# Kernel tuning notes

Measured on AMD Instinct MI355X. Metric: run time of the kernel, lower is better.

Reference implementation:

```python
import jax, jax.numpy as jnp
import numpy as np

HEADS = 16
HEAD_DIM = 128
LAMBDA_INIT = 0.8
RMS_EPS = 1.1920928955078125e-07  # torch.finfo(float32).eps (RMSNorm eps=None default)


def setup_inputs() -> dict:
    key = jax.random.key(0)
    ks = jax.random.split(key, 9)
    b, s, d = 2, 2048, 2048
    x = jax.random.normal(ks[0], (b, s, d), dtype=jnp.float32)
    # torch Linear weights are (out_features, in_features); apply as x @ W.T
    wq = jax.random.normal(ks[1], (d, d), dtype=jnp.float32) * 0.02
    wk = jax.random.normal(ks[2], (d, d), dtype=jnp.float32) * 0.02
    wv = jax.random.normal(ks[3], (d, d), dtype=jnp.float32) * 0.02
    wo = jax.random.normal(ks[4], (d, d), dtype=jnp.float32) * 0.02
    # lambda vectors scaled small so exp(dot) stays finite
    lambda_q1 = jax.random.normal(ks[5], (HEAD_DIM,), dtype=jnp.float32) * 0.1
    lambda_q2 = jax.random.normal(ks[6], (HEAD_DIM,), dtype=jnp.float32) * 0.1
    lambda_k1 = jax.random.normal(ks[7], (HEAD_DIM,), dtype=jnp.float32) * 0.1
    lambda_k2 = jax.random.normal(ks[8], (HEAD_DIM,), dtype=jnp.float32) * 0.1
    return {"x": x, "wq": wq, "wk": wk, "wv": wv, "wo": wo,
            "lambda_q1": lambda_q1, "lambda_q2": lambda_q2,
            "lambda_k1": lambda_k1, "lambda_k2": lambda_k2}


def reference(x, wq, wk, wv, wo, lambda_q1, lambda_q2, lambda_k1, lambda_k2):
    b, s, d = x.shape
    h, hd = HEADS, HEAD_DIM
    # projections -> (b, h, s, hd)
    q = (x @ wq.T).reshape(b, s, h, hd).transpose(0, 2, 1, 3)
    k = (x @ wk.T).reshape(b, s, h, hd).transpose(0, 2, 1, 3)
    v = (x @ wv.T).reshape(b, s, h, hd).transpose(0, 2, 1, 3)
    q1, q2 = jnp.split(q, 2, axis=-1)
    k1, k2 = jnp.split(k, 2, axis=-1)
    # NOTE: source scales by sqrt(full head_dim), not the chunked dim
    scale = 1.0 / jnp.sqrt(jnp.float32(hd))
    a1 = jax.nn.softmax(jnp.einsum('bhqd,bhkd->bhqk', q1, k1) * scale, axis=-1)
    a2 = jax.nn.softmax(jnp.einsum('bhqd,bhkd->bhqk', q2, k2) * scale, axis=-1)
    lam = jnp.exp(jnp.dot(lambda_q1, lambda_k1)) - jnp.exp(jnp.dot(lambda_q2, lambda_k2)) + LAMBDA_INIT
    out = jnp.einsum('bhqk,bhkd->bhqd', a1 - lam * a2, v)  # (b,h,s,hd)
    # per-head RMSNorm (no affine) scaled by (1 - lambda_init)
    rms = jnp.sqrt(jnp.mean(out * out, axis=-1, keepdims=True) + RMS_EPS)
    normed = out / rms * (1.0 - LAMBDA_INIT)
    # faithful to torch: cat over heads on dim 1 -> (b, h*s, hd),
    # transpose(1,2) -> (b, hd, h*s), contiguous view -> (b, s, d)
    t = normed.reshape(b, h * s, hd).transpose(0, 2, 1).reshape(b, s, d)
    return t @ wo.T
```

## Files before the change

### kernel.cpp

```cpp
#include <hip/hip_runtime.h>
#include <hip/hip_bf16.h>
#include <cstdint>
#include <cstddef>

typedef __attribute__((ext_vector_type(8))) short short8;
typedef __attribute__((ext_vector_type(4))) float f4;
typedef __attribute__((ext_vector_type(4))) int i4;

#define MFMA16(a, b, c) __builtin_amdgcn_mfma_f32_16x16x32_bf16((a), (b), (c), 0, 0, 0)

__device__ __forceinline__ float bf2f(unsigned short u) {
    union { unsigned int i; float f; } v; v.i = ((unsigned int)u) << 16; return v.f;
}
__device__ __forceinline__ unsigned short f2bf(float f) {
    union { float f; unsigned int i; } v; v.f = f;
    unsigned int x = v.i;
    x += 0x7fffu + ((x >> 16) & 1u);
    return (unsigned short)(x >> 16);
}
__device__ __forceinline__ i4 pack8(const float* p) {
    f4 v0 = *(const f4*)p;
    f4 v1 = *(const f4*)(p + 4);
    unsigned int w0 = (unsigned int)f2bf(v0[0]) | ((unsigned int)f2bf(v0[1]) << 16);
    unsigned int w1 = (unsigned int)f2bf(v0[2]) | ((unsigned int)f2bf(v0[3]) << 16);
    unsigned int w2 = (unsigned int)f2bf(v1[0]) | ((unsigned int)f2bf(v1[1]) << 16);
    unsigned int w3 = (unsigned int)f2bf(v1[2]) | ((unsigned int)f2bf(v1[3]) << 16);
    i4 r; r[0] = (int)w0; r[1] = (int)w1; r[2] = (int)w2; r[3] = (int)w3; return r;
}

static constexpr int S = 2048;
static constexpr int D = 2048;
static constexpr int H = 16;
static constexpr int HD = 128;
static constexpr int B = 2;

__global__ void detect_kernel(const unsigned short* __restrict__ w,
                              const void* __restrict__ lq1, const void* __restrict__ lq2,
                              const void* __restrict__ lk1, const void* __restrict__ lk2,
                              int* __restrict__ ctrl) {
    const int lane = threadIdx.x;
    int hits = 0;
    for (int j = 0; j < 4; j++) {
        unsigned short u = w[lane * 4 + j];
        hits += (((u >> 7) & 0xFF) >= 134) ? 1 : 0;
    }
    for (int m = 1; m <= 32; m <<= 1) hits += __shfl_xor(hits, m, 64);
    const int flag = (hits >= 16) ? 1 : 0;

    float d1 = 0.f, d2 = 0.f;
    for (int t = 0; t < 2; t++) {
        int e = lane + t * 64;
        float q1v, k1v, q2v, k2v;
        if (flag) {
            q1v = ((const float*)lq1)[e]; k1v = ((const float*)lk1)[e];
            q2v = ((const float*)lq2)[e]; k2v = ((const float*)lk2)[e];
        } else {
            q1v = bf2f(((const unsigned short*)lq1)[e]); k1v = bf2f(((const unsigned short*)lk1)[e]);
            q2v = bf2f(((const unsigned short*)lq2)[e]); k2v = bf2f(((const unsigned short*)lk2)[e]);
        }
        d1 += q1v * k1v; d2 += q2v * k2v;
    }
    for (int m = 1; m <= 32; m <<= 1) { d1 += __shfl_xor(d1, m, 64); d2 += __shfl_xor(d2, m, 64); }
    if (lane == 0) {
        ctrl[0] = flag;
        ctrl[1] = __float_as_int(__expf(d1) - __expf(d2) + 0.8f);
    }
}

__global__ __launch_bounds__(256) void proj_kernel(
    const void* __restrict__ Xr,
    const void* __restrict__ Wqr, const void* __restrict__ Wkr, const void* __restrict__ Wvr,
    const int* __restrict__ ctrl,
    unsigned short* __restrict__ Qb,
    unsigned short* __restrict__ Kb,
    unsigned short* __restrict__ Vt)
{
    const int flag = ctrl[0];
    const int zm = blockIdx.z;
    const void* __restrict__ Wr = (zm == 0) ? Wqr : ((zm == 1) ? Wkr : Wvr);
    const int bm = blockIdx.x, bn = blockIdx.y;
    const int K = D;

    __shared__ __align__(16) unsigned short As[64 * 32];
    __shared__ __align__(16) unsigned short Bs[64 * 32];

    const int tid  = threadIdx.x;
    const int lane = tid & 63;
    const int wave = tid >> 6;
    const int quad = lane >> 4;
    const int l16  = lane & 15;
    const int wm   = (wave >> 1) * 32;
    const int wn   = (wave & 1) * 32;
    const int arow  = tid >> 2;
    const int akoff = (tid & 3) * 8;

    f4 acc[2][2] = {};

    for (int k0 = 0; k0 < K; k0 += 32) {
        size_t xi = (size_t)(bm * 64 + arow) * K + k0 + akoff;
        size_t wi = (size_t)(bn * 64 + arow) * K + k0 + akoff;
        __syncthreads();
        if (flag) {
            *(i4*)&As[arow * 32 + akoff] = pack8(&((const float*)Xr)[xi]);
            *(i4*)&Bs[arow * 32 + akoff] = pack8(&((const float*)Wr)[wi]);
        } else {
            *(i4*)&As[arow * 32 + akoff] = *(const i4*)&((const unsigned short*)Xr)[xi];
            *(i4*)&Bs[arow * 32 + akoff] = *(const i4*)&((const unsigned short*)Wr)[wi];
        }
        __syncthreads();

        short8 a0 = *(const short8*)&As[(wm + l16) * 32 + quad * 8];
        short8 a1 = *(const short8*)&As[(wm + 16 + l16) * 32 + quad * 8];
        short8 b0 = *(const short8*)&Bs[(wn + l16) * 32 + quad * 8];
        short8 b1 = *(const short8*)&Bs[(wn + 16 + l16) * 32 + quad * 8];

        acc[0][0] = MFMA16(a0, b0, acc[0][0]);
        acc[0][1] = MFMA16(a0, b1, acc[0][1]);
        acc[1][0] = MFMA16(a1, b0, acc[1][0]);
        acc[1][1] = MFMA16(a1, b1, acc[1][1]);
    }

    for (int r = 0; r < 2; r++)
        for (int c = 0; c < 2; c++)
            for (int reg = 0; reg < 4; reg++) {
                int row = bm * 64 + wm + r * 16 + quad * 4 + reg;
                int col = bn * 64 + wn + c * 16 + l16;
                int b_idx = row >> 11, s0 = row & (S - 1);
                int h0 = col >> 7, e = col & (HD - 1);
                unsigned short val = f2bf(acc[r][c][reg]);
                if (zm == 2) {
                    Vt[(((size_t)(b_idx * H + h0)) * HD + e) * S + s0] = val;
                } else {
                    unsigned short* O = (zm == 0) ? Qb : Kb;
                    O[(((size_t)(b_idx * H + h0)) * S + s0) * HD + e] = val;
                }
            }
}

__global__ __launch_bounds__(256) void attn_kernel(
    const unsigned short* __restrict__ Qb,
    const unsigned short* __restrict__ Kb,
    const unsigned short* __restrict__ Vt,
    const int* __restrict__ ctrl,
    unsigned short* __restrict__ Nm)
{
    const int h = blockIdx.y, b = blockIdx.z;
    const unsigned short* __restrict__ q  = Qb + ((size_t)(b * H + h)) * S * HD;
    const unsigned short* __restrict__ k  = Kb + ((size_t)(b * H + h)) * S * HD;
    const unsigned short* __restrict__ vt = Vt + ((size_t)(b * H + h)) * HD * S;
    const float lam = __int_as_float(ctrl[1]);

    const int tid  = threadIdx.x;
    const int lane = tid & 63;
    const int wave = tid >> 6;
    const int quad = lane >> 4;
    const int l16  = lane & 15;
    const int row0 = blockIdx.x * 64 + wave * 16;

    short8 aq1[2], aq2[2];
    for (int t = 0; t < 2; t++) {
        aq1[t] = *(const short8*)&q[((size_t)(row0 + l16)) * HD + t * 32 + quad * 8];
        aq2[t] = *(const short8*)&q[((size_t)(row0 + l16)) * HD + 64 + t * 32 + quad * 8];
    }

    __shared__ __align__(16) unsigned short plds[4][2][16 * 32];

    float l1[4] = {}, l2[4] = {};
    f4 o1[8] = {}, o2[8] = {};

    const float scale = 0.08838834764831845f;

    for (int key0 = 0; key0 < S; key0 += 32) {
        f4 s1a = {}, s1b = {}, s2a = {}, s2b = {};
        for (int t = 0; t < 2; t++) {
            short8 b1a = *(const short8*)&k[((size_t)(key0 + l16)) * HD + t * 32 + quad * 8];
            short8 b1b = *(const short8*)&k[((size_t)(key0 + 16 + l16)) * HD + t * 32 + quad * 8];
            short8 b2a = *(const short8*)&k[((size_t)(key0 + l16)) * HD + 64 + t * 32 + quad * 8];
            short8 b2b = *(const short8*)&k[((size_t)(key0 + 16 + l16)) * HD + 64 + t * 32 + quad * 8];
            s1a = MFMA16(aq1[t], b1a, s1a);
            s1b = MFMA16(aq1[t], b1b, s1b);
            s2a = MFMA16(aq2[t], b2a, s2a);
            s2b = MFMA16(aq2[t], b2b, s2b);
        }

        unsigned short* pl1 = plds[wave][0];
        unsigned short* pl2 = plds[wave][1];
        #pragma unroll
        for (int r = 0; r < 4; r++) {
            float pa1 = __expf(s1a[r] * scale);
            float pb1 = __expf(s1b[r] * scale);
            float pa2 = __expf(s2a[r] * scale);
            float pb2 = __expf(s2b[r] * scale);
            pl1[(quad * 4 + r) * 32 + l16]      = f2bf(pa1);
            pl1[(quad * 4 + r) * 32 + 16 + l16] = f2bf(pb1);
            pl2[(quad * 4 + r) * 32 + l16]      = f2bf(pa2);
            pl2[(quad * 4 + r) * 32 + 16 + l16] = f2bf(pb2);
            float rs1 = pa1 + pb1;
            float rs2 = pa2 + pb2;
            for (int mask = 1; mask <= 8; mask <<= 1) {
                rs1 += __shfl_xor(rs1, mask, 64);
                rs2 += __shfl_xor(rs2, mask, 64);
            }
            l1[r] += rs1;
            l2[r] += rs2;
        }
        __syncthreads();

        short8 ap1 = *(const short8*)&pl1[l16 * 32 + quad * 8];
        short8 ap2 = *(const short8*)&pl2[l16 * 32 + quad * 8];
        #pragma unroll
        for (int f = 0; f < 8; f++) {
            short8 bv = *(const short8*)&vt[((size_t)(f * 16 + l16)) * S + key0 + quad * 8];
            o1[f] = MFMA16(ap1, bv, o1[f]);
            o2[f] = MFMA16(ap2, bv, o2[f]);
        }
        __syncthreads();
    }

    float ssq[4] = {};
    for (int f = 0; f < 8; f++)
        for (int r = 0; r < 4; r++) {
            float fin = o1[f][r] / l1[r] - lam * (o2[f][r] / l2[r]);
            o1[f][r] = fin;
            ssq[r] += fin * fin;
        }
    for (int r = 0; r < 4; r++)
        for (int mask = 1; mask <= 8; mask <<= 1)
            ssq[r] += __shfl_xor(ssq[r], mask, 64);

    for (int r = 0; r < 4; r++) {
        float rms = sqrtf(ssq[r] * (1.0f / 128.0f) + 1.1920928955078125e-07f);
        float sc = 0.2f / rms;
        int s0 = row0 + quad * 4 + r;
        for (int f = 0; f < 8; f++) {
            int e = f * 16 + l16;
            Nm[((size_t)b * D + (e * H + h)) * S + s0] = f2bf(o1[f][r] * sc);
        }
    }
}

__global__ __launch_bounds__(256) void out_kernel(
    const unsigned short* __restrict__ Nm,
    const void* __restrict__ Wor,
    const int* __restrict__ ctrl,
    void* __restrict__ Out)
{
    const int flag = ctrl[0];
    const int bz = blockIdx.z;
    const unsigned short* __restrict__ A = Nm + (size_t)bz * D * S;
    const int K = S;
    const int bm = blockIdx.x, bn = blockIdx.y;

    __shared__ __align__(16) unsigned short As[64 * 32];
    __shared__ __align__(16) unsigned short Bs[64 * 32];

    const int tid  = threadIdx.x;
    const int lane = tid & 63;
    const int wave = tid >> 6;
    const int quad = lane >> 4;
    const int l16  = lane & 15;
    const int wm   = (wave >> 1) * 32;
    const int wn   = (wave & 1) * 32;
    const int arow  = tid >> 2;
    const int akoff = (tid & 3) * 8;

    f4 acc[2][2] = {};

    for (int k0 = 0; k0 < K; k0 += 32) {
        size_t ai = (size_t)(bm * 64 + arow) * K + k0 + akoff;
        size_t wi = (size_t)(bn * 64 + arow) * K + k0 + akoff;
        __syncthreads();
        *(i4*)&As[arow * 32 + akoff] = *(const i4*)&A[ai];
        if (flag) *(i4*)&Bs[arow * 32 + akoff] = pack8(&((const float*)Wor)[wi]);
        else      *(i4*)&Bs[arow * 32 + akoff] = *(const i4*)&((const unsigned short*)Wor)[wi];
        __syncthreads();

        short8 a0 = *(const short8*)&As[(wm + l16) * 32 + quad * 8];
        short8 a1 = *(const short8*)&As[(wm + 16 + l16) * 32 + quad * 8];
        short8 b0 = *(const short8*)&Bs[(wn + l16) * 32 + quad * 8];
        short8 b1 = *(const short8*)&Bs[(wn + 16 + l16) * 32 + quad * 8];

        acc[0][0] = MFMA16(a0, b0, acc[0][0]);
        acc[0][1] = MFMA16(a0, b1, acc[0][1]);
        acc[1][0] = MFMA16(a1, b0, acc[1][0]);
        acc[1][1] = MFMA16(a1, b1, acc[1][1]);
    }

    for (int r = 0; r < 2; r++)
        for (int c = 0; c < 2; c++)
            for (int reg = 0; reg < 4; reg++) {
                int row = bm * 64 + wm + r * 16 + quad * 4 + reg;
                int col = bn * 64 + wn + c * 16 + l16;
                size_t idx = (size_t)bz * S * D + (size_t)row * D + col;
                if (flag) ((float*)Out)[idx] = acc[r][c][reg];
                else      ((unsigned short*)Out)[idx] = f2bf(acc[r][c][reg]);
            }
}

static constexpr size_t NEED_BYTES = 256 + 4ull * 8 * 1024 * 1024 * 2;
static void* g_extra = nullptr;

extern "C" void kernel_launch(void* const* d_in, const int* in_sizes, int n_in,
                              void* d_out, int out_size, void* d_ws, size_t ws_size,
                              hipStream_t stream) {
    const void* x   = d_in[0];
    const void* wq  = d_in[1];
    const void* wk  = d_in[2];
    const void* wv  = d_in[3];
    const void* wo  = d_in[4];
    const void* lq1 = d_in[5];
    const void* lq2 = d_in[6];
    const void* lk1 = d_in[7];
    const void* lk2 = d_in[8];

    char* base;
    if (ws_size >= NEED_BYTES) {
        base = (char*)d_ws;
    } else {
        if (!g_extra) (void)hipMalloc(&g_extra, NEED_BYTES);
        base = g_extra ? (char*)g_extra : (char*)d_ws;
    }

    int* ctrl = (int*)base;
    unsigned short* pw = (unsigned short*)(base + 256);
    const size_t NH = (size_t)B * H * S * HD;
    unsigned short* Qb = pw;            pw += NH;
    unsigned short* Kb = pw;            pw += NH;
    unsigned short* Vt = pw;            pw += NH;
    unsigned short* Nm = pw;

    detect_kernel<<<1, 64, 0, stream>>>((const unsigned short*)wq, lq1, lq2, lk1, lk2, ctrl);

    dim3 g1(64, 32, 3);
    proj_kernel<<<g1, 256, 0, stream>>>(x, wq, wk, wv, ctrl, Qb, Kb, Vt);

    dim3 g2(S / 64, H, B);
    attn_kernel<<<g2, 256, 0, stream>>>(Qb, Kb, Vt, ctrl, Nm);

    dim3 g3(32, 32, B);
    out_kernel<<<g3, 256, 0, stream>>>(Nm, wo, ctrl, d_out);
}
```

Baseline: 999.1 us.

## Pre-convert inputs to bf16, enlarge GEMM tiles, use direct-to-LDS loads, pipeline attention loads

Adds conversion kernels that turn x and all weights into bf16 buffers once per call, so the GEMMs no longer convert fp32 to bf16 inside their inner loop. Both projection GEMMs move from 64x64 to 128x128 block tiles with 4x4 MFMA per wave and fill shared memory with global_load_lds. The attention kernel double-buffers K/V register fragments across two 32-key steps, packs the P stores into 32-bit writes, drops the per-step block barriers, and defers the row-sum shuffles to the end. The cost is extra workspace and conversion traffic, more registers per wave, and far fewer blocks in the output GEMM grid.

```diff
diff --git a/kernel.cpp b/kernel.cpp
--- a/kernel.cpp
+++ b/kernel.cpp
@@ -26,6 +26,12 @@
     unsigned int w2 = (unsigned int)f2bf(v1[0]) | ((unsigned int)f2bf(v1[1]) << 16);
     unsigned int w3 = (unsigned int)f2bf(v1[2]) | ((unsigned int)f2bf(v1[3]) << 16);
     i4 r; r[0] = (int)w0; r[1] = (int)w1; r[2] = (int)w2; r[3] = (int)w3; return r;
+}
+__device__ __forceinline__ void g2l16(const unsigned short* g, unsigned short* l) {
+    __builtin_amdgcn_global_load_lds(
+        (const __attribute__((address_space(1))) unsigned int*)g,
+        (__attribute__((address_space(3))) unsigned int*)l,
+        16, 0, 0);
 }
 
 static constexpr int S = 2048;
@@ -67,67 +73,76 @@
     }
 }
 
+__global__ __launch_bounds__(256) void conv_kernel(const void* __restrict__ src,
+                                                   unsigned short* __restrict__ dst,
+                                                   int n, const int* __restrict__ ctrl) {
+    int i = (blockIdx.x * 256 + threadIdx.x) * 8;
+    if (i >= n) return;
+    if (ctrl[0]) *(i4*)&dst[i] = pack8(&((const float*)src)[i]);
+    else         *(i4*)&dst[i] = *(const i4*)&((const unsigned short*)src)[i];
+}
+
 __global__ __launch_bounds__(256) void proj_kernel(
-    const void* __restrict__ Xr,
-    const void* __restrict__ Wqr, const void* __restrict__ Wkr, const void* __restrict__ Wvr,
-    const int* __restrict__ ctrl,
+    const unsigned short* __restrict__ X,
+    const unsigned short* __restrict__ Wq, const unsigned short* __restrict__ Wk,
+    const unsigned short* __restrict__ Wv,
     unsigned short* __restrict__ Qb,
     unsigned short* __restrict__ Kb,
     unsigned short* __restrict__ Vt)
 {
-    const int flag = ctrl[0];
     const int zm = blockIdx.z;
-    const void* __restrict__ Wr = (zm == 0) ? Wqr : ((zm == 1) ? Wkr : Wvr);
+    const unsigned short* __restrict__ W = (zm == 0) ? Wq : ((zm == 1) ? Wk : Wv);
     const int bm = blockIdx.x, bn = blockIdx.y;
     const int K = D;
 
-    __shared__ __align__(16) unsigned short As[64 * 32];
-    __shared__ __align__(16) unsigned short Bs[64 * 32];
+    __shared__ __align__(16) unsigned short As[128 * 32];
+    __shared__ __align__(16) unsigned short Bs[128 * 32];
 
     const int tid  = threadIdx.x;
     const int lane = tid & 63;
     const int wave = tid >> 6;
     const int quad = lane >> 4;
     const int l16  = lane & 15;
-    const int wm   = (wave >> 1) * 32;
-    const int wn   = (wave & 1) * 32;
-    const int arow  = tid >> 2;
-    const int akoff = (tid & 3) * 8;
-
-    f4 acc[2][2] = {};
+    const int wm   = (wave >> 1) * 64;
+    const int wn   = (wave & 1) * 64;
+    const int r0   = tid >> 2;
+    const int koff = (tid & 3) * 8;
+
+    f4 acc[4][4] = {};
 
     for (int k0 = 0; k0 < K; k0 += 32) {
-        size_t xi = (size_t)(bm * 64 + arow) * K + k0 + akoff;
-        size_t wi = (size_t)(bn * 64 + arow) * K + k0 + akoff;
         __syncthreads();
-        if (flag) {
-            *(i4*)&As[arow * 32 + akoff] = pack8(&((const float*)Xr)[xi]);
-            *(i4*)&Bs[arow * 32 + akoff] = pack8(&((const float*)Wr)[wi]);
-        } else {
-            *(i4*)&As[arow * 32 + akoff] = *(const i4*)&((const unsigned short*)Xr)[xi];
-            *(i4*)&Bs[arow * 32 + akoff] = *(const i4*)&((const unsigned short*)Wr)[wi];
-        }
+        g2l16(&X[(size_t)(bm * 128 + r0) * K + k0 + koff],
+              (unsigned short*)((char*)As + wave * 1024));
+        g2l16(&X[(size_t)(bm * 128 + r0 + 64) * K + k0 + koff],
+              (unsigned short*)((char*)As + wave * 1024 + 4096));
+        g2l16(&W[(size_t)(bn * 128 + r0) * K + k0 + koff],
+              (unsigned short*)((char*)Bs + wave * 1024));
+        g2l16(&W[(size_t)(bn * 128 + r0 + 64) * K + k0 + koff],
+              (unsigned short*)((char*)Bs + wave * 1024 + 4096));
         __syncthreads();
 
-        short8 a0 = *(const short8*)&As[(wm + l16) * 32 + quad * 8];
-        short8 a1 = *(const short8*)&As[(wm + 16 + l16) * 32 + quad * 8];
-        short8 b0 = *(const short8*)&Bs[(wn + l16) * 32 + quad * 8];
-        short8 b1 = *(const short8*)&Bs[(wn + 16 + l16) * 32 + quad * 8];
-
-        acc[0][0] = MFMA16(a0, b0, acc[0][0]);
-        acc[0][1] = MFMA16(a0, b1, acc[0][1]);
-        acc[1][0] = MFMA16(a1, b0, acc[1][0]);
-        acc[1][1] = MFMA16(a1, b1, acc[1][1]);
-    }
-
-    for (int r = 0; r < 2; r++)
-        for (int c = 0; c < 2; c++)
+        short8 a[4], b[4];
+        #pragma unroll
+        for (int i = 0; i < 4; i++) {
+            a[i] = *(const short8*)&As[(wm + i * 16 + l16) * 32 + quad * 8];
+            b[i] = *(const short8*)&Bs[(wn + i * 16 + l16) * 32 + quad * 8];
+        }
+        #pragma unroll
+        for (int i = 0; i < 4; i++)
+            #pragma unroll
+            for (int j = 0; j < 4; j++)
+                acc[i][j] = MFMA16(a[i], b[j], acc[i][j]);
+    }
+
+    for (int i = 0; i < 4; i++)
+        for (int j = 0; j < 4; j++)
             for (int reg = 0; reg < 4; reg++) {
-                int row = bm * 64 + wm + r * 16 + quad * 4 + reg;
-                int col = bn * 64 + wn + c * 16 + l16;
+                int row = bm * 128 + wm + i * 16 + quad * 4 + reg;
+                int col = bn * 128 + wn + j * 16 + l16;
                 int b_idx = row >> 11, s0 = row & (S - 1);
                 int h0 = col >> 7, e = col & (HD - 1);
-                unsigned short val = f2bf(acc[r][c][reg]);
+                unsigned short val = f2bf(acc[i][j][reg]);
                 if (zm == 2) {
                     Vt[(((size_t)(b_idx * H + h0)) * HD + e) * S + s0] = val;
                 } else {
@@ -137,7 +152,7 @@
             }
 }
 
-__global__ __launch_bounds__(256) void attn_kernel(
+__global__ __launch_bounds__(256, 2) void attn_kernel(
     const unsigned short* __restrict__ Qb,
     const unsigned short* __restrict__ Kb,
     const unsigned short* __restrict__ Vt,
@@ -158,6 +173,7 @@
     const int row0 = blockIdx.x * 64 + wave * 16;
 
     short8 aq1[2], aq2[2];
+    #pragma unroll
     for (int t = 0; t < 2; t++) {
         aq1[t] = *(const short8*)&q[((size_t)(row0 + l16)) * HD + t * 32 + quad * 8];
         aq2[t] = *(const short8*)&q[((size_t)(row0 + l16)) * HD + 64 + t * 32 + quad * 8];
@@ -167,55 +183,73 @@
 
     float l1[4] = {}, l2[4] = {};
     f4 o1[8] = {}, o2[8] = {};
-
     const float scale = 0.08838834764831845f;
 
-    for (int key0 = 0; key0 < S; key0 += 32) {
-        f4 s1a = {}, s1b = {}, s2a = {}, s2b = {};
-        for (int t = 0; t < 2; t++) {
-            short8 b1a = *(const short8*)&k[((size_t)(key0 + l16)) * HD + t * 32 + quad * 8];
-            short8 b1b = *(const short8*)&k[((size_t)(key0 + 16 + l16)) * HD + t * 32 + quad * 8];
-            short8 b2a = *(const short8*)&k[((size_t)(key0 + l16)) * HD + 64 + t * 32 + quad * 8];
-            short8 b2b = *(const short8*)&k[((size_t)(key0 + 16 + l16)) * HD + 64 + t * 32 + quad * 8];
-            s1a = MFMA16(aq1[t], b1a, s1a);
-            s1b = MFMA16(aq1[t], b1b, s1b);
-            s2a = MFMA16(aq2[t], b2a, s2a);
-            s2b = MFMA16(aq2[t], b2b, s2b);
-        }
-
-        unsigned short* pl1 = plds[wave][0];
-        unsigned short* pl2 = plds[wave][1];
-        #pragma unroll
-        for (int r = 0; r < 4; r++) {
-            float pa1 = __expf(s1a[r] * scale);
-            float pb1 = __expf(s1b[r] * scale);
-            float pa2 = __expf(s2a[r] * scale);
-            float pb2 = __expf(s2b[r] * scale);
-            pl1[(quad * 4 + r) * 32 + l16]      = f2bf(pa1);
-            pl1[(quad * 4 + r) * 32 + 16 + l16] = f2bf(pb1);
-            pl2[(quad * 4 + r) * 32 + l16]      = f2bf(pa2);
-            pl2[(quad * 4 + r) * 32 + 16 + l16] = f2bf(pb2);
-            float rs1 = pa1 + pb1;
-            float rs2 = pa2 + pb2;
-            for (int mask = 1; mask <= 8; mask <<= 1) {
-                rs1 += __shfl_xor(rs1, mask, 64);
-                rs2 += __shfl_xor(rs2, mask, 64);
-            }
-            l1[r] += rs1;
-            l2[r] += rs2;
-        }
-        __syncthreads();
-
-        short8 ap1 = *(const short8*)&pl1[l16 * 32 + quad * 8];
-        short8 ap2 = *(const short8*)&pl2[l16 * 32 + quad * 8];
-        #pragma unroll
-        for (int f = 0; f < 8; f++) {
-            short8 bv = *(const short8*)&vt[((size_t)(f * 16 + l16)) * S + key0 + quad * 8];
-            o1[f] = MFMA16(ap1, bv, o1[f]);
-            o2[f] = MFMA16(ap2, bv, o2[f]);
-        }
-        __syncthreads();
-    }
+    unsigned short* pl1 = &plds[wave][0][0];
+    unsigned short* pl2 = &plds[wave][1][0];
+
+    #define LOADK(key0, kf)                                                              \
+        {                                                                                \
+            _Pragma("unroll") for (int v = 0; v < 2; v++)                                \
+            _Pragma("unroll") for (int st = 0; st < 2; st++)                             \
+            _Pragma("unroll") for (int t = 0; t < 2; t++)                                \
+                kf[v][st][t] = *(const short8*)&k[(size_t)((key0) + 2 * l16 + st) * HD   \
+                                                  + v * 64 + t * 32 + quad * 8];         \
+        }
+    #define LOADV(key0, vf)                                                              \
+        {                                                                                \
+            _Pragma("unroll") for (int f = 0; f < 8; f++)                                \
+                vf[f] = *(const short8*)&vt[(size_t)(f * 16 + l16) * S + (key0) + quad * 8]; \
+        }
+    #define BODY(key0, kf, vf)                                                           \
+        {                                                                                \
+            f4 s1a = {}, s1b = {}, s2a = {}, s2b = {};                                   \
+            _Pragma("unroll") for (int t = 0; t < 2; t++) {                              \
+                s1a = MFMA16(aq1[t], kf[0][0][t], s1a);                                  \
+                s1b = MFMA16(aq1[t], kf[0][1][t], s1b);                                  \
+                s2a = MFMA16(aq2[t], kf[1][0][t], s2a);                                  \
+                s2b = MFMA16(aq2[t], kf[1][1][t], s2b);                                  \
+            }                                                                            \
+            _Pragma("unroll") for (int r = 0; r < 4; r++) {                              \
+                float pa1 = __expf(s1a[r] * scale);                                      \
+                float pb1 = __expf(s1b[r] * scale);                                      \
+                float pa2 = __expf(s2a[r] * scale);                                      \
+                float pb2 = __expf(s2b[r] * scale);                                      \
+                *(unsigned int*)&pl1[(quad * 4 + r) * 32 + 2 * l16] =                    \
+                    (unsigned int)f2bf(pa1) | ((unsigned int)f2bf(pb1) << 16);           \
+                *(unsigned int*)&pl2[(quad * 4 + r) * 32 + 2 * l16] =                    \
+                    (unsigned int)f2bf(pa2) | ((unsigned int)f2bf(pb2) << 16);           \
+                l1[r] += pa1 + pb1;                                                      \
+                l2[r] += pa2 + pb2;                                                      \
+            }                                                                            \
+            short8 ap1 = *(const short8*)&pl1[l16 * 32 + quad * 8];                      \
+            short8 ap2 = *(const short8*)&pl2[l16 * 32 + quad * 8];                      \
+            _Pragma("unroll") for (int f = 0; f < 8; f++) {                              \
+                o1[f] = MFMA16(ap1, vf[f], o1[f]);                                       \
+                o2[f] = MFMA16(ap2, vf[f], o2[f]);                                       \
+            }                                                                            \
+        }
+
+    short8 kA[2][2][2], kB[2][2][2], vA[8], vB[8];
+    LOADK(0, kA); LOADV(0, vA);
+
+    for (int key0 = 0; key0 < S; key0 += 64) {
+        LOADK(key0 + 32, kB); LOADV(key0 + 32, vB);
+        BODY(key0, kA, vA);
+        int nx = (key0 + 64 < S) ? key0 + 64 : 0;
+        LOADK(nx, kA); LOADV(nx, vA);
+        BODY(key0 + 32, kB, vB);
+    }
+    #undef LOADK
+    #undef LOADV
+    #undef BODY
+
+    #pragma unroll
+    for (int r = 0; r < 4; r++)
+        for (int mask = 1; mask <= 8; mask <<= 1) {
+            l1[r] += __shfl_xor(l1[r], mask, 64);
+            l2[r] += __shfl_xor(l2[r], mask, 64);
+        }
 
     float ssq[4] = {};
     for (int f = 0; f < 8; f++)
@@ -241,7 +275,7 @@
 
 __global__ __launch_bounds__(256) void out_kernel(
     const unsigned short* __restrict__ Nm,
-    const void* __restrict__ Wor,
+    const unsigned short* __restrict__ Wo,
     const int* __restrict__ ctrl,
     void* __restrict__ Out)
 {
@@ -251,53 +285,58 @@
     const int K = S;
     const int bm = blockIdx.x, bn = blockIdx.y;
 
-    __shared__ __align__(16) unsigned short As[64 * 32];
-    __shared__ __align__(16) unsigned short Bs[64 * 32];
+    __shared__ __align__(16) unsigned short As[128 * 32];
+    __shared__ __align__(16) unsigned short Bs[128 * 32];
 
     const int tid  = threadIdx.x;
     const int lane = tid & 63;
     const int wave = tid >> 6;
     const int quad = lane >> 4;
     const int l16  = lane & 15;
-    const int wm   = (wave >> 1) * 32;
-    const int wn   = (wave & 1) * 32;
-    const int arow  = tid >> 2;
-    const int akoff = (tid & 3) * 8;
-
-    f4 acc[2][2] = {};
+    const int wm   = (wave >> 1) * 64;
+    const int wn   = (wave & 1) * 64;
+    const int r0   = tid >> 2;
+    const int koff = (tid & 3) * 8;
+
+    f4 acc[4][4] = {};
 
     for (int k0 = 0; k0 < K; k0 += 32) {
-        size_t ai = (size_t)(bm * 64 + arow) * K + k0 + akoff;
-        size_t wi = (size_t)(bn * 64 + arow) * K + k0 + akoff;
         __syncthreads();
-        *(i4*)&As[arow * 32 + akoff] = *(const i4*)&A[ai];
-        if (flag) *(i4*)&Bs[arow * 32 + akoff] = pack8(&((const float*)Wor)[wi]);
-        else      *(i4*)&Bs[arow * 32 + akoff] = *(const i4*)&((const unsigned short*)Wor)[wi];
+        g2l16(&A[(size_t)(bm * 128 + r0) * K + k0 + koff],
+              (unsigned short*)((char*)As + wave * 1024));
+        g2l16(&A[(size_t)(bm * 128 + r0 + 64) * K + k0 + koff],
+              (unsigned short*)((char*)As + wave * 1024 + 4096));
+        g2l16(&Wo[(size_t)(bn * 128 + r0) * K + k0 + koff],
+              (unsigned short*)((char*)Bs + wave * 1024));
+        g2l16(&Wo[(size_t)(bn * 128 + r0 + 64) * K + k0 + koff],
+              (unsigned short*)((char*)Bs + wave * 1024 + 4096));
         __syncthreads();
 
-        short8 a0 = *(const short8*)&As[(wm + l16) * 32 + quad * 8];
-        short8 a1 = *(const short8*)&As[(wm + 16 + l16) * 32 + quad * 8];
-        short8 b0 = *(const short8*)&Bs[(wn + l16) * 32 + quad * 8];
-        short8 b1 = *(const short8*)&Bs[(wn + 16 + l16) * 32 + quad * 8];
-
-        acc[0][0] = MFMA16(a0, b0, acc[0][0]);
-        acc[0][1] = MFMA16(a0, b1, acc[0][1]);
-        acc[1][0] = MFMA16(a1, b0, acc[1][0]);
-        acc[1][1] = MFMA16(a1, b1, acc[1][1]);
-    }
-
-    for (int r = 0; r < 2; r++)
-        for (int c = 0; c < 2; c++)
+        short8 a[4], b[4];
+        #pragma unroll
+        for (int i = 0; i < 4; i++) {
+            a[i] = *(const short8*)&As[(wm + i * 16 + l16) * 32 + quad * 8];
+            b[i] = *(const short8*)&Bs[(wn + i * 16 + l16) * 32 + quad * 8];
+        }
+        #pragma unroll
+        for (int i = 0; i < 4; i++)
+            #pragma unroll
+            for (int j = 0; j < 4; j++)
+                acc[i][j] = MFMA16(a[i], b[j], acc[i][j]);
+    }
+
+    for (int i = 0; i < 4; i++)
+        for (int j = 0; j < 4; j++)
             for (int reg = 0; reg < 4; reg++) {
-                int row = bm * 64 + wm + r * 16 + quad * 4 + reg;
-                int col = bn * 64 + wn + c * 16 + l16;
+                int row = bm * 128 + wm + i * 16 + quad * 4 + reg;
+                int col = bn * 128 + wn + j * 16 + l16;
                 size_t idx = (size_t)bz * S * D + (size_t)row * D + col;
-                if (flag) ((float*)Out)[idx] = acc[r][c][reg];
-                else      ((unsigned short*)Out)[idx] = f2bf(acc[r][c][reg]);
+                if (flag) ((float*)Out)[idx] = acc[i][j][reg];
+                else      ((unsigned short*)Out)[idx] = f2bf(acc[i][j][reg]);
             }
 }
 
-static constexpr size_t NEED_BYTES = 256 + 4ull * 8 * 1024 * 1024 * 2;
+static constexpr size_t NEED_BYTES = 256 + 56ull * 1024 * 1024 * 2;
 static void* g_extra = nullptr;
 
 extern "C" void kernel_launch(void* const* d_in, const int* in_sizes, int n_in,
@@ -323,20 +362,33 @@
 
     int* ctrl = (int*)base;
     unsigned short* pw = (unsigned short*)(base + 256);
+    const size_t NX = (size_t)B * S * D;
+    const size_t NW = (size_t)D * D;
     const size_t NH = (size_t)B * H * S * HD;
-    unsigned short* Qb = pw;            pw += NH;
-    unsigned short* Kb = pw;            pw += NH;
-    unsigned short* Vt = pw;            pw += NH;
-    unsigned short* Nm = pw;
+    unsigned short* Xc  = pw;  pw += NX;
+    unsigned short* Wqc = pw;  pw += NW;
+    unsigned short* Wkc = pw;  pw += NW;
+    unsigned short* Wvc = pw;  pw += NW;
+    unsigned short* Woc = pw;  pw += NW;
+    unsigned short* Qb  = pw;  pw += NH;
+    unsigned short* Kb  = pw;  pw += NH;
+    unsigned short* Vt  = pw;  pw += NH;
+    unsigned short* Nm  = pw;
 
     detect_kernel<<<1, 64, 0, stream>>>((const unsigned short*)wq, lq1, lq2, lk1, lk2, ctrl);
 
-    dim3 g1(64, 32, 3);
-    proj_kernel<<<g1, 256, 0, stream>>>(x, wq, wk, wv, ctrl, Qb, Kb, Vt);
+    conv_kernel<<<(int)(NX / 2048), 256, 0, stream>>>(x,  Xc,  (int)NX, ctrl);
+    conv_kernel<<<(int)(NW / 2048), 256, 0, stream>>>(wq, Wqc, (int)NW, ctrl);
+    conv_kernel<<<(int)(NW / 2048), 256, 0, stream>>>(wk, Wkc, (int)NW, ctrl);
+    conv_kernel<<<(int)(NW / 2048), 256, 0, stream>>>(wv, Wvc, (int)NW, ctrl);
+    conv_kernel<<<(int)(NW / 2048), 256, 0, stream>>>(wo, Woc, (int)NW, ctrl);
+
+    dim3 g1(32, 16, 3);
+    proj_kernel<<<g1, 256, 0, stream>>>(Xc, Wqc, Wkc, Wvc, Qb, Kb, Vt);
 
     dim3 g2(S / 64, H, B);
     attn_kernel<<<g2, 256, 0, stream>>>(Qb, Kb, Vt, ctrl, Nm);
 
-    dim3 g3(32, 32, B);
-    out_kernel<<<g3, 256, 0, stream>>>(Nm, wo, ctrl, d_out);
-}
+    dim3 g3(16, 16, 2);
+    out_kernel<<<g3, 256, 0, stream>>>(Nm, Woc, ctrl, d_out);
+}
```

New measurement: 807.0 us. -19.2%, faster.
